# Performance work log

Measured on AMD Instinct MI355X. Metric: run time of the kernel, lower is better.

## Reference

```python
import jax, jax.numpy as jnp
import numpy as np
import math

B, S, D = 4096, 16, 256
HS, HT, O = 512, 512, 1


def setup_inputs() -> dict:
    key = jax.random.key(0)
    ks = jax.random.split(key, 20)
    stdv_s = 1.0 / math.sqrt(HS)
    stdv_t = 1.0 / math.sqrt(HT)
    u = lambda k, shape, s: jax.random.uniform(k, shape, jnp.float32, -s, s)
    return {
        "X": jax.random.normal(ks[0], (B, S, D), jnp.float32),
        # SpatialLSTM params (init uniform(-1/sqrt(H), 1/sqrt(H)) as in torch)
        "sa_W": u(ks[1], (D, 4 * HS), stdv_s),
        "sa_U": u(ks[2], (HS, 4 * HS), stdv_s),
        "sa_b": u(ks[3], (4 * HS,), stdv_s),
        "sa_Wa": u(ks[4], (D, D), stdv_s),
        "sa_Ua": u(ks[5], (2 * HS, D), stdv_s),
        "sa_ba": u(ks[6], (D,), stdv_s),
        "sa_Va": u(ks[7], (D, D), stdv_s),
        # TemporalLSTM params
        "ta_Wa": u(ks[8], (HS, S), stdv_t),
        "ta_Ua": u(ks[9], (HT, S), stdv_t),
        "ta_ba": u(ks[10], (S,), stdv_t),
        "ta_Va": u(ks[11], (S, S), stdv_t),
        "ta_W": u(ks[12], (HS, 4 * HT), stdv_t),
        "ta_U": u(ks[13], (HT, 4 * HT), stdv_t),
        "ta_b": u(ks[14], (4 * HT,), stdv_t),
        "ta_Wy": u(ks[15], (O, 4 * HT), stdv_t),
        "fc_W": u(ks[16], (O, HT), stdv_t),
        "fc_b": u(ks[17], (O,), stdv_t),
    }


def _lstm_update(gates, c, H):
    i = jax.nn.sigmoid(gates[:, :H])
    f = jax.nn.sigmoid(gates[:, H:2 * H])
    g = jnp.tanh(gates[:, 2 * H:3 * H])
    o = jax.nn.sigmoid(gates[:, 3 * H:])
    c_new = f * c + i * g
    h_new = o * jnp.tanh(c_new)
    return h_new, c_new


def _forward(X, sa_W, sa_U, sa_b, sa_Wa, sa_Ua, sa_ba, sa_Va,
             ta_Wa, ta_Ua, ta_ba, ta_Va, ta_W, ta_U, ta_b, ta_Wy, fc_W, fc_b):
    batch = X.shape[0]
    x = X  # x = X[:, :, 0:input_dim] == full X
    y0 = X[:, 0, D - 1:D]  # y = X[:, :, input_dim-1:], take t=0 -> [B, 1]

    # ---- Spatial attention LSTM over time ----
    def sa_step(carry, x_t):
        h, c = carry
        hc = jnp.concatenate([h, c], axis=1)  # [B, 2*HS]
        a_t = jnp.tanh(x_t @ sa_Wa + hc @ sa_Ua + sa_ba) @ sa_Va  # [B, D]
        alpha_t = jax.nn.softmax(a_t, axis=1)
        xt = alpha_t * x_t
        gates = xt @ sa_W + h @ sa_U + sa_b  # [B, 4*HS]
        h, c = _lstm_update(gates, c, HS)
        return (h, c), h

    h0 = jnp.zeros((batch, HS), X.dtype)
    c0 = jnp.zeros((batch, HS), X.dtype)
    _, hseq = jax.lax.scan(sa_step, (h0, c0), jnp.swapaxes(x, 0, 1))  # [S, B, HS]
    H3 = jnp.swapaxes(hseq, 0, 1)  # [B, S, HS]

    # ---- Temporal attention LSTM ----
    s0 = jnp.zeros((batch, HT), X.dtype)  # s_t is never updated in the original code

    def ta_step(carry, h_t):
        lh, lc, y_prev = carry
        beta = jnp.tanh(h_t @ ta_Wa + s0 @ ta_Ua + ta_ba) @ ta_Va  # [B, S]
        beta = jax.nn.softmax(beta, axis=1)
        h_ctx = jnp.einsum('bs,bsh->bh', beta, H3)  # [B, HS]
        gates = h_ctx @ ta_W + lh @ ta_U + y_prev @ ta_Wy + ta_b  # [B, 4*HT]
        lh, lc = _lstm_update(gates, lc, HT)
        y = lh @ fc_W.T + fc_b  # [B, O]
        return (lh, lc, y), None

    (_, _, y_pred), _ = jax.lax.scan(ta_step, (h0[:, :HT] * 0.0, c0[:, :HT] * 0.0, y0), hseq)
    return y_pred  # [B, O]


def reference(X, sa_W, sa_U, sa_b, sa_Wa, sa_Ua, sa_ba, sa_Va,
              ta_Wa, ta_Ua, ta_ba, ta_Va, ta_W, ta_U, ta_b, ta_Wy, fc_W, fc_b):
    return _forward(X, sa_W, sa_U, sa_b, sa_Wa, sa_Ua, sa_ba, sa_Va,
                    ta_Wa, ta_Ua, ta_ba, ta_Va, ta_W, ta_U, ta_b, ta_Wy, fc_W, fc_b)
```

## Files before the change

kernel.cpp:

```cpp
#include <hip/hip_runtime.h>


constexpr int Bb = 4096;
constexpr int Ss = 16;
constexpr int Dd = 256;
constexpr int Hh = 512;

typedef __attribute__((ext_vector_type(8))) short short8;
typedef __attribute__((ext_vector_type(4))) float f32x4;

__device__ __forceinline__ float sigm(float x) { return 1.0f / (1.0f + expf(-x)); }

__device__ __forceinline__ unsigned short f2bf(float x) {
    unsigned int u = __float_as_uint(x);
    u = (u + 0x7fffu + ((u >> 16) & 1u)) >> 16;
    return (unsigned short)u;
}
__device__ __forceinline__ float bf2f(unsigned short h) {
    return __uint_as_float(((unsigned int)h) << 16);
}
__device__ __forceinline__ void async16(const void* g, void* l) {
    __builtin_amdgcn_global_load_lds(
        (const __attribute__((address_space(1))) void*)g,
        (__attribute__((address_space(3))) void*)l, 16, 0, 0);
}

struct SegB { const unsigned short* Ah; const unsigned short* Al;
              const unsigned short* Bh; const unsigned short* Bl;
              int lda; int ldb; int K; };

template<int BM, int BN, int NSEG, int EPI>
__global__ __launch_bounds__(256) void gemm_mfma_k(
    SegB s0, SegB s1, SegB s2,
    const float* __restrict__ bias,
    float* __restrict__ C,
    unsigned short* __restrict__ Th, unsigned short* __restrict__ Tl,
    int ldc)
{
    constexpr int WM = BM / 2, WN = BN / 2;
    constexpr int FI = WM / 16, FJ = WN / 16;
    __shared__ __align__(16) unsigned short sA[2][BM * 32];
    __shared__ __align__(16) unsigned short sB[2][BN * 32];
    const int tid  = threadIdx.x;
    const int lane = tid & 63;
    const int wv   = tid >> 6;
    const int wm   = wv & 1, wn = wv >> 1;
    const int row0 = blockIdx.x * BM;
    const int col0 = blockIdx.y * BN;

    f32x4 acc[FI][FJ];
#pragma unroll
    for (int i = 0; i < FI; i++)
#pragma unroll
        for (int j = 0; j < FJ; j++) acc[i][j] = (f32x4){0.f, 0.f, 0.f, 0.f};

    const int lrow = lane >> 2;
    const int lcol = (lane & 3) * 8;
    const int q8   = (lane >> 4) * 8;
    const int l15  = lane & 15;

#pragma unroll
    for (int sgi = 0; sgi < NSEG; ++sgi) {
        const SegB sg = (sgi == 0) ? s0 : ((sgi == 1) ? s1 : s2);
        const int K = sg.K;
        for (int k0 = 0; k0 < K; k0 += 32) {
#pragma unroll
            for (int c = wv; c < BM / 16; c += 4) {
                const int r = c * 16 + lrow;
                const size_t gA = (size_t)(row0 + r) * sg.lda + k0 + lcol;
                const int lo = c * 512 + lane * 8;
                async16(sg.Ah + gA, &sA[0][lo]);
                async16(sg.Al + gA, &sA[1][lo]);
            }
#pragma unroll
            for (int c = wv; c < BN / 16; c += 4) {
                const int r = c * 16 + lrow;
                const size_t gB = (size_t)(col0 + r) * sg.ldb + k0 + lcol;
                const int lo = c * 512 + lane * 8;
                async16(sg.Bh + gB, &sB[0][lo]);
                async16(sg.Bl + gB, &sB[1][lo]);
            }
            __syncthreads();
            short8 ah[FI], al[FI], bh[FJ], bl[FJ];
#pragma unroll
            for (int i = 0; i < FI; i++) {
                const int m = wm * WM + i * 16 + l15;
                ah[i] = *reinterpret_cast<const short8*>(&sA[0][m * 32 + q8]);
                al[i] = *reinterpret_cast<const short8*>(&sA[1][m * 32 + q8]);
            }
#pragma unroll
            for (int j = 0; j < FJ; j++) {
                const int n = wn * WN + j * 16 + l15;
                bh[j] = *reinterpret_cast<const short8*>(&sB[0][n * 32 + q8]);
                bl[j] = *reinterpret_cast<const short8*>(&sB[1][n * 32 + q8]);
            }
#pragma unroll
            for (int i = 0; i < FI; i++)
#pragma unroll
                for (int j = 0; j < FJ; j++) {
                    acc[i][j] = __builtin_amdgcn_mfma_f32_16x16x32_bf16(ah[i], bh[j], acc[i][j], 0, 0, 0);
                    acc[i][j] = __builtin_amdgcn_mfma_f32_16x16x32_bf16(ah[i], bl[j], acc[i][j], 0, 0, 0);
                    acc[i][j] = __builtin_amdgcn_mfma_f32_16x16x32_bf16(al[i], bh[j], acc[i][j], 0, 0, 0);
                }
            __syncthreads();
        }
    }
#pragma unroll
    for (int i = 0; i < FI; i++) {
#pragma unroll
        for (int j = 0; j < FJ; j++) {
            const int col = col0 + wn * WN + j * 16 + l15;
#pragma unroll
            for (int r = 0; r < 4; r++) {
                const int row = row0 + wm * WM + i * 16 + (lane >> 4) * 4 + r;
                float v = acc[i][j][r];
                if (EPI == 1) {
                    v = tanhf(v + bias[col]);
                    unsigned short hb = f2bf(v);
                    Th[(size_t)row * ldc + col] = hb;
                    Tl[(size_t)row * ldc + col] = f2bf(v - bf2f(hb));
                } else {
                    C[(size_t)row * ldc + col] = v;
                }
            }
        }
    }
}

template<int NSEG, int ZC, int TA>
__global__ __launch_bounds__(256) void gemm_gates_k(
    SegB s0, SegB s1,
    const float* __restrict__ bias,
    const float* __restrict__ wy,
    const float* __restrict__ yv,
    float* __restrict__ c_io,
    unsigned short* __restrict__ hh, unsigned short* __restrict__ hl,
    unsigned short* __restrict__ ch, unsigned short* __restrict__ cl)
{
    __shared__ __align__(16) unsigned short sA[2][128 * 32];
    __shared__ __align__(16) unsigned short sB[2][128 * 32];
    const int tid  = threadIdx.x;
    const int lane = tid & 63;
    const int wv   = tid >> 6;
    const int wm   = wv & 1, wn = wv >> 1;
    const int row0 = blockIdx.x * 128;
    const int by32 = blockIdx.y * 32;

    f32x4 acc[4][4];
#pragma unroll
    for (int i = 0; i < 4; i++)
#pragma unroll
        for (int g = 0; g < 4; g++) acc[i][g] = (f32x4){0.f, 0.f, 0.f, 0.f};

    const int lrow = lane >> 2;
    const int lcol = (lane & 3) * 8;
    const int q8   = (lane >> 4) * 8;
    const int l15  = lane & 15;

#pragma unroll
    for (int sgi = 0; sgi < NSEG; ++sgi) {
        const SegB sg = (sgi == 0) ? s0 : s1;
        const int K = sg.K;
        for (int k0 = 0; k0 < K; k0 += 32) {
#pragma unroll
            for (int c = wv; c < 8; c += 4) {
                const int r = c * 16 + lrow;
                const size_t gA = (size_t)(row0 + r) * sg.lda + k0 + lcol;
                const int lo = c * 512 + lane * 8;
                async16(sg.Ah + gA, &sA[0][lo]);
                async16(sg.Al + gA, &sA[1][lo]);
            }
#pragma unroll
            for (int cc = wv; cc < 8; cc += 4) {
                const int g  = cc >> 1;
                const int jj = (cc & 1) * 16 + lrow;
                const int rowg = g * 512 + by32 + jj;
                const size_t gB = (size_t)rowg * sg.ldb + k0 + lcol;
                const int lo = cc * 512 + lane * 8;
                async16(sg.Bh + gB, &sB[0][lo]);
                async16(sg.Bl + gB, &sB[1][lo]);
            }
            __syncthreads();
            short8 ah[4], al[4], bh[4], bl[4];
#pragma unroll
            for (int i = 0; i < 4; i++) {
                const int m = wm * 64 + i * 16 + l15;
                ah[i] = *reinterpret_cast<const short8*>(&sA[0][m * 32 + q8]);
                al[i] = *reinterpret_cast<const short8*>(&sA[1][m * 32 + q8]);
            }
#pragma unroll
            for (int g = 0; g < 4; g++) {
                const int n = g * 32 + wn * 16 + l15;
                bh[g] = *reinterpret_cast<const short8*>(&sB[0][n * 32 + q8]);
                bl[g] = *reinterpret_cast<const short8*>(&sB[1][n * 32 + q8]);
            }
#pragma unroll
            for (int i = 0; i < 4; i++)
#pragma unroll
                for (int g = 0; g < 4; g++) {
                    acc[i][g] = __builtin_amdgcn_mfma_f32_16x16x32_bf16(ah[i], bh[g], acc[i][g], 0, 0, 0);
                    acc[i][g] = __builtin_amdgcn_mfma_f32_16x16x32_bf16(ah[i], bl[g], acc[i][g], 0, 0, 0);
                    acc[i][g] = __builtin_amdgcn_mfma_f32_16x16x32_bf16(al[i], bh[g], acc[i][g], 0, 0, 0);
                }
            __syncthreads();
        }
    }
    const int j = by32 + wn * 16 + l15;
    const float b0 = bias[j],            b1 = bias[Hh + j];
    const float b2 = bias[2 * Hh + j],   b3 = bias[3 * Hh + j];
    float w0 = 0.f, w1 = 0.f, w2 = 0.f, w3 = 0.f;
    if (TA) { w0 = wy[j]; w1 = wy[Hh + j]; w2 = wy[2 * Hh + j]; w3 = wy[3 * Hh + j]; }
#pragma unroll
    for (int i = 0; i < 4; i++) {
        const int rbase = row0 + wm * 64 + i * 16 + (lane >> 4) * 4;
#pragma unroll
        for (int r = 0; r < 4; r++) {
            const int row = rbase + r;
            float gi = acc[i][0][r] + b0;
            float gf = acc[i][1][r] + b1;
            float gg = acc[i][2][r] + b2;
            float go = acc[i][3][r] + b3;
            if (TA) {
                const float yb = yv[row];
                gi += yb * w0; gf += yb * w1; gg += yb * w2; go += yb * w3;
            }
            const float i_ = sigm(gi), f_ = sigm(gf), gv = tanhf(gg), o_ = sigm(go);
            const size_t idx = (size_t)row * Hh + j;
            const float cp = ZC ? 0.0f : c_io[idx];
            const float c = f_ * cp + i_ * gv;
            c_io[idx] = c;
            const float h = o_ * tanhf(c);
            const unsigned short hb = f2bf(h);
            hh[idx] = hb;
            hl[idx] = f2bf(h - bf2f(hb));
            if (!TA) {
                const unsigned short cb = f2bf(c);
                ch[idx] = cb;
                cl[idx] = f2bf(c - bf2f(cb));
            }
        }
    }
}

__global__ __launch_bounds__(256) void splitT_k(const float* __restrict__ W,
                                                unsigned short* __restrict__ Th,
                                                unsigned short* __restrict__ Tl,
                                                int Kd, int Nd)
{
    __shared__ float tile[32][33];
    const int bk = blockIdx.x * 32, bn = blockIdx.y * 32;
    const int tid = threadIdx.x;
    const int r = tid >> 3, c4 = (tid & 7) * 4;
    const float4 v = *reinterpret_cast<const float4*>(&W[(size_t)(bk + r) * Nd + bn + c4]);
    tile[r][c4 + 0] = v.x; tile[r][c4 + 1] = v.y;
    tile[r][c4 + 2] = v.z; tile[r][c4 + 3] = v.w;
    __syncthreads();
    const int n = r, k4 = c4;
    ushort4 hq, lq;
    unsigned short* hp = (unsigned short*)&hq;
    unsigned short* lp = (unsigned short*)&lq;
#pragma unroll
    for (int q = 0; q < 4; q++) {
        float x = tile[k4 + q][n];
        unsigned short h = f2bf(x);
        hp[q] = h;
        lp[q] = f2bf(x - bf2f(h));
    }
    *reinterpret_cast<ushort4*>(&Th[(size_t)(bn + n) * Kd + bk + k4]) = hq;
    *reinterpret_cast<ushort4*>(&Tl[(size_t)(bn + n) * Kd + bk + k4]) = lq;
}

__global__ __launch_bounds__(256) void splitWa_k(const float* __restrict__ W,
                                                 unsigned short* __restrict__ Th,
                                                 unsigned short* __restrict__ Tl)
{
    int idx = blockIdx.x * 256 + threadIdx.x;
    int n = idx >> 9, k = idx & 511;
    float x = W[(size_t)k * 16 + n];
    unsigned short h = f2bf(x);
    Th[idx] = h;
    Tl[idx] = f2bf(x - bf2f(h));
}

__global__ __launch_bounds__(256) void init_k(const float* __restrict__ X,
                                              unsigned short* __restrict__ xsh,
                                              unsigned short* __restrict__ xsl,
                                              float* __restrict__ yv)
{
    int idx = blockIdx.x * 256 + threadIdx.x;
    int b = idx >> 8, d = idx & 255;
    float xv = X[(size_t)b * (Ss * Dd) + d];
    unsigned short hb = f2bf(xv);
    xsh[idx] = hb;
    xsl[idx] = f2bf(xv - bf2f(hb));
    if (d == Dd - 1) yv[b] = xv;
}

template<int SPLITX>
__global__ __launch_bounds__(256) void softmax_xt_k(const float* __restrict__ a,
                                                    const float* __restrict__ X,
                                                    unsigned short* __restrict__ xh,
                                                    unsigned short* __restrict__ xl,
                                                    unsigned short* __restrict__ xsh,
                                                    unsigned short* __restrict__ xsl,
                                                    int t)
{
    int b = blockIdx.x, tid = threadIdx.x;
    __shared__ float red[256];
    float v = a[(size_t)b * Dd + tid];
    red[tid] = v; __syncthreads();
    for (int s = 128; s > 0; s >>= 1) {
        if (tid < s) red[tid] = fmaxf(red[tid], red[tid + s]);
        __syncthreads();
    }
    float mx = red[0]; __syncthreads();
    float e = expf(v - mx);
    red[tid] = e; __syncthreads();
    for (int s = 128; s > 0; s >>= 1) {
        if (tid < s) red[tid] += red[tid + s];
        __syncthreads();
    }
    float inv = 1.0f / red[0];
    float xv = e * inv * X[(size_t)b * Ss * Dd + (size_t)t * Dd + tid];
    unsigned short h = f2bf(xv);
    xh[(size_t)b * Dd + tid] = h;
    xl[(size_t)b * Dd + tid] = f2bf(xv - bf2f(h));
    if (SPLITX) {
        float xn = X[(size_t)b * Ss * Dd + (size_t)(t + 1) * Dd + tid];
        unsigned short xb = f2bf(xn);
        xsh[(size_t)b * Dd + tid] = xb;
        xsl[(size_t)b * Dd + tid] = f2bf(xn - bf2f(xb));
    }
}

__global__ __launch_bounds__(256) void beta_k(const unsigned short* __restrict__ H3h,
                                              const unsigned short* __restrict__ H3l,
                                              const unsigned short* __restrict__ WaTh,
                                              const unsigned short* __restrict__ WaTl,
                                              const float* __restrict__ taba,
                                              const float* __restrict__ taVa,
                                              float* __restrict__ beta)
{
    __shared__ __align__(16) unsigned short sW[2][16 * 512];
    __shared__ __align__(16) unsigned short sA[2][128 * 32];
    __shared__ float tt[128][17];
    __shared__ float Vas[256];
    const int tid  = threadIdx.x;
    const int lane = tid & 63;
    const int wv   = tid >> 6;
    const int lrow = lane >> 2;
    const int lcol = (lane & 3) * 8;
    const int q8   = (lane >> 4) * 8;
    const int l15  = lane & 15;
    const size_t row0 = (size_t)blockIdx.x * 128;

#pragma unroll
    for (int it = 0; it < 4; ++it) {
        const int lo = wv * 2048 + it * 512 + lane * 8;
        async16(WaTh + lo, &sW[0][lo]);
        async16(WaTl + lo, &sW[1][lo]);
    }
    Vas[tid] = taVa[tid];

    f32x4 acc[2];
    acc[0] = (f32x4){0.f, 0.f, 0.f, 0.f};
    acc[1] = (f32x4){0.f, 0.f, 0.f, 0.f};

    for (int kc = 0; kc < 16; ++kc) {
        const int k0 = kc * 32;
#pragma unroll
        for (int c = wv; c < 8; c += 4) {
            const int r = c * 16 + lrow;
            const size_t gA = (row0 + r) * Hh + k0 + lcol;
            const int lo = c * 512 + lane * 8;
            async16(H3h + gA, &sA[0][lo]);
            async16(H3l + gA, &sA[1][lo]);
        }
        __syncthreads();
        const short8 bh = *reinterpret_cast<const short8*>(&sW[0][l15 * 512 + k0 + q8]);
        const short8 bl = *reinterpret_cast<const short8*>(&sW[1][l15 * 512 + k0 + q8]);
#pragma unroll
        for (int i = 0; i < 2; i++) {
            const int m = wv * 32 + i * 16 + l15;
            const short8 ah = *reinterpret_cast<const short8*>(&sA[0][m * 32 + q8]);
            const short8 al = *reinterpret_cast<const short8*>(&sA[1][m * 32 + q8]);
            acc[i] = __builtin_amdgcn_mfma_f32_16x16x32_bf16(ah, bh, acc[i], 0, 0, 0);
            acc[i] = __builtin_amdgcn_mfma_f32_16x16x32_bf16(ah, bl, acc[i], 0, 0, 0);
            acc[i] = __builtin_amdgcn_mfma_f32_16x16x32_bf16(al, bh, acc[i], 0, 0, 0);
        }
        __syncthreads();
    }
    const float ba = taba[l15];
#pragma unroll
    for (int i = 0; i < 2; i++) {
#pragma unroll
        for (int r = 0; r < 4; r++) {
            const int rl = wv * 32 + i * 16 + (lane >> 4) * 4 + r;
            tt[rl][l15] = tanhf(acc[i][r] + ba);
        }
    }
    __syncthreads();
    if (tid < 128) {
        float tv[16];
#pragma unroll
        for (int m = 0; m < 16; m++) tv[m] = tt[tid][m];
        float l[16];
        float mx = -1e30f;
#pragma unroll
        for (int n = 0; n < 16; n++) {
            float s = 0.0f;
#pragma unroll
            for (int m = 0; m < 16; m++) s = fmaf(tv[m], Vas[m * 16 + n], s);
            l[n] = s;
            mx = fmaxf(mx, s);
        }
        float sum = 0.0f;
#pragma unroll
        for (int n = 0; n < 16; n++) { l[n] = expf(l[n] - mx); sum += l[n]; }
        const float inv = 1.0f / sum;
        float* bp = beta + (row0 + tid) * 16;
#pragma unroll
        for (int n4 = 0; n4 < 4; n4++) {
            float4 v = { l[n4 * 4] * inv, l[n4 * 4 + 1] * inv,
                         l[n4 * 4 + 2] * inv, l[n4 * 4 + 3] * inv };
            *reinterpret_cast<float4*>(bp + n4 * 4) = v;
        }
    }
}

__global__ __launch_bounds__(256) void hctx_all_k(unsigned short* __restrict__ H3h,
                                                  unsigned short* __restrict__ H3l,
                                                  const float* __restrict__ beta)
{
    const int b = blockIdx.x, tid = threadIdx.x;
    __shared__ float4 Hs4[16][129];
    __shared__ float bs[16][16];
    for (int i = tid; i < 16 * 128; i += 256) {
        const int s = i >> 7, q = i & 127;
        const size_t o = ((size_t)s * Bb + b) * Hh + q * 4;
        const ushort4 hv = *reinterpret_cast<const ushort4*>(&H3h[o]);
        const ushort4 lv = *reinterpret_cast<const ushort4*>(&H3l[o]);
        Hs4[s][q] = (float4){ bf2f(hv.x) + bf2f(lv.x), bf2f(hv.y) + bf2f(lv.y),
                              bf2f(hv.z) + bf2f(lv.z), bf2f(hv.w) + bf2f(lv.w) };
    }
    {
        const int t = tid >> 4, s = tid & 15;
        bs[t][s] = beta[((size_t)t * Bb + b) * 16 + s];
    }
    __syncthreads();
    const int q  = tid & 127;
    const int t0 = tid >> 7;
#pragma unroll
    for (int tt = 0; tt < 8; tt++) {
        const int t = tt * 2 + t0;
        float4 a = (float4){0.f, 0.f, 0.f, 0.f};
#pragma unroll
        for (int s = 0; s < 16; s++) {
            const float w = bs[t][s];
            const float4 hv = Hs4[s][q];
            a.x = fmaf(w, hv.x, a.x); a.y = fmaf(w, hv.y, a.y);
            a.z = fmaf(w, hv.z, a.z); a.w = fmaf(w, hv.w, a.w);
        }
        ushort4 ho, lo;
        ho.x = f2bf(a.x); lo.x = f2bf(a.x - bf2f(ho.x));
        ho.y = f2bf(a.y); lo.y = f2bf(a.y - bf2f(ho.y));
        ho.z = f2bf(a.z); lo.z = f2bf(a.z - bf2f(ho.z));
        ho.w = f2bf(a.w); lo.w = f2bf(a.w - bf2f(ho.w));
        const size_t o = ((size_t)t * Bb + b) * Hh + q * 4;
        *reinterpret_cast<ushort4*>(&H3h[o]) = ho;
        *reinterpret_cast<ushort4*>(&H3l[o]) = lo;
    }
}

__global__ __launch_bounds__(256) void y_k(const unsigned short* __restrict__ hh,
                                           const unsigned short* __restrict__ hl,
                                           const float* __restrict__ fcW,
                                           const float* __restrict__ fcb,
                                           float* __restrict__ yv,
                                           float* __restrict__ outp)
{
    int b = blockIdx.x, tid = threadIdx.x;
    size_t o = (size_t)b * Hh + tid;
    float h0 = bf2f(hh[o]) + bf2f(hl[o]);
    float h1 = bf2f(hh[o + 256]) + bf2f(hl[o + 256]);
    float p = h0 * fcW[tid] + h1 * fcW[tid + 256];
#pragma unroll
    for (int off = 32; off > 0; off >>= 1) p += __shfl_down(p, off, 64);
    __shared__ float wred[4];
    if ((tid & 63) == 0) wred[tid >> 6] = p;
    __syncthreads();
    if (tid == 0) {
        float y = fcb[0] + wred[0] + wred[1] + wred[2] + wred[3];
        yv[b] = y;
        if (outp) outp[b] = y;
    }
}

extern "C" void kernel_launch(void* const* d_in, const int* in_sizes, int n_in,
                              void* d_out, int out_size, void* d_ws, size_t ws_size,
                              hipStream_t stream)
{
    (void)in_sizes; (void)n_in; (void)out_size; (void)ws_size;
    const float* X     = (const float*)d_in[0];
    const float* sa_W  = (const float*)d_in[1];
    const float* sa_U  = (const float*)d_in[2];
    const float* sa_b  = (const float*)d_in[3];
    const float* sa_Wa = (const float*)d_in[4];
    const float* sa_Ua = (const float*)d_in[5];
    const float* sa_ba = (const float*)d_in[6];
    const float* sa_Va = (const float*)d_in[7];
    const float* ta_Wa = (const float*)d_in[8];
    const float* ta_ba = (const float*)d_in[10];
    const float* ta_Va = (const float*)d_in[11];
    const float* ta_W  = (const float*)d_in[12];
    const float* ta_U  = (const float*)d_in[13];
    const float* ta_b  = (const float*)d_in[14];
    const float* ta_Wy = (const float*)d_in[15];
    const float* fc_W  = (const float*)d_in[16];
    const float* fc_b  = (const float*)d_in[17];

    char* base = (char*)d_ws;
    size_t off = 0;
    auto alloc = [&](size_t bytes) {
        void* p = base + off; off += (bytes + 255) & ~(size_t)255; return p;
    };
    const size_t BH = (size_t)Bb * Hh;
    float* avxt = (float*)alloc((size_t)Bb * Dd * 4);
    unsigned short* H3h = (unsigned short*)alloc((size_t)Ss * BH * 2);
    unsigned short* H3l = (unsigned short*)alloc((size_t)Ss * BH * 2);
    float* cbuf = (float*)alloc(BH * 4);
    float* lc   = (float*)alloc(BH * 4);
    unsigned short* lhBh = (unsigned short*)alloc(BH * 2);
    unsigned short* lhBl = (unsigned short*)alloc(BH * 2);
    unsigned short* xth = (unsigned short*)alloc((size_t)Bb * Dd * 2);
    unsigned short* xtl = (unsigned short*)alloc((size_t)Bb * Dd * 2);
    unsigned short* xsh = (unsigned short*)alloc((size_t)Bb * Dd * 2);
    unsigned short* xsl = (unsigned short*)alloc((size_t)Bb * Dd * 2);
    unsigned short* ch  = (unsigned short*)alloc(BH * 2);
    unsigned short* cl  = (unsigned short*)alloc(BH * 2);
    unsigned short* tmph = (unsigned short*)alloc((size_t)Bb * Dd * 2);
    unsigned short* tmpl = (unsigned short*)alloc((size_t)Bb * Dd * 2);
    unsigned short* saWth = (unsigned short*)alloc((size_t)Dd * 4 * Hh * 2);
    unsigned short* saWtl = (unsigned short*)alloc((size_t)Dd * 4 * Hh * 2);
    unsigned short* saUth = (unsigned short*)alloc((size_t)Hh * 4 * Hh * 2);
    unsigned short* saUtl = (unsigned short*)alloc((size_t)Hh * 4 * Hh * 2);
    unsigned short* taWth = (unsigned short*)alloc((size_t)Hh * 4 * Hh * 2);
    unsigned short* taWtl = (unsigned short*)alloc((size_t)Hh * 4 * Hh * 2);
    unsigned short* taUth = (unsigned short*)alloc((size_t)Hh * 4 * Hh * 2);
    unsigned short* taUtl = (unsigned short*)alloc((size_t)Hh * 4 * Hh * 2);
    unsigned short* WaTh = (unsigned short*)alloc((size_t)Dd * Dd * 2);
    unsigned short* WaTl = (unsigned short*)alloc((size_t)Dd * Dd * 2);
    unsigned short* UaTh = (unsigned short*)alloc((size_t)2 * Hh * Dd * 2);
    unsigned short* UaTl = (unsigned short*)alloc((size_t)2 * Hh * Dd * 2);
    unsigned short* VaTh = (unsigned short*)alloc((size_t)Dd * Dd * 2);
    unsigned short* VaTl = (unsigned short*)alloc((size_t)Dd * Dd * 2);
    unsigned short* tWaTh = (unsigned short*)alloc((size_t)16 * Hh * 2);
    unsigned short* tWaTl = (unsigned short*)alloc((size_t)16 * Hh * 2);
    float* yv = (float*)alloc((size_t)Bb * 4);
    float* beta = (float*)xth;
    unsigned short* lhAh = (unsigned short*)cbuf;
    unsigned short* lhAl = (unsigned short*)cbuf + BH;
    unsigned short* lhh[2] = { lhAh, lhBh };
    unsigned short* lhl[2] = { lhAl, lhBl };

    splitT_k<<<dim3(Dd / 32, (4 * Hh) / 32), 256, 0, stream>>>(sa_W, saWth, saWtl, Dd, 4 * Hh);
    splitT_k<<<dim3(Hh / 32, (4 * Hh) / 32), 256, 0, stream>>>(sa_U, saUth, saUtl, Hh, 4 * Hh);
    splitT_k<<<dim3(Hh / 32, (4 * Hh) / 32), 256, 0, stream>>>(ta_W, taWth, taWtl, Hh, 4 * Hh);
    splitT_k<<<dim3(Hh / 32, (4 * Hh) / 32), 256, 0, stream>>>(ta_U, taUth, taUtl, Hh, 4 * Hh);
    splitT_k<<<dim3(Dd / 32, Dd / 32), 256, 0, stream>>>(sa_Wa, WaTh, WaTl, Dd, Dd);
    splitT_k<<<dim3((2 * Hh) / 32, Dd / 32), 256, 0, stream>>>(sa_Ua, UaTh, UaTl, 2 * Hh, Dd);
    splitT_k<<<dim3(Dd / 32, Dd / 32), 256, 0, stream>>>(sa_Va, VaTh, VaTl, Dd, Dd);
    splitWa_k<<<dim3(32), 256, 0, stream>>>(ta_Wa, tWaTh, tWaTl);
    init_k<<<dim3((Bb * Dd) / 256), 256, 0, stream>>>(X, xsh, xsl, yv);

    const dim3 agrid(Bb / 32, Dd / 64);
    const dim3 ggrid(Bb / 128, Hh / 32);

    for (int t = 0; t < Ss; ++t) {
        SegB a0{ xsh, xsl, WaTh, WaTl, Dd, Dd, Dd };
        if (t == 0) {
            gemm_mfma_k<32, 64, 1, 1><<<agrid, 256, 0, stream>>>(
                a0, a0, a0, sa_ba, nullptr, tmph, tmpl, Dd);
        } else {
            SegB a1{ H3h + (size_t)(t - 1) * BH, H3l + (size_t)(t - 1) * BH,
                     UaTh, UaTl, Hh, 2 * Hh, Hh };
            SegB a2{ ch, cl, UaTh + Hh, UaTl + Hh, Hh, 2 * Hh, Hh };
            gemm_mfma_k<32, 64, 3, 1><<<agrid, 256, 0, stream>>>(
                a0, a1, a2, sa_ba, nullptr, tmph, tmpl, Dd);
        }

        SegB v0{ tmph, tmpl, VaTh, VaTl, Dd, Dd, Dd };
        gemm_mfma_k<32, 64, 1, 0><<<agrid, 256, 0, stream>>>(
            v0, v0, v0, nullptr, avxt, nullptr, nullptr, Dd);

        if (t < Ss - 1)
            softmax_xt_k<1><<<Bb, 256, 0, stream>>>(avxt, X, xth, xtl, xsh, xsl, t);
        else
            softmax_xt_k<0><<<Bb, 256, 0, stream>>>(avxt, X, xth, xtl, xsh, xsl, t);

        SegB g0{ xth, xtl, saWth, saWtl, Dd, Dd, Dd };
        if (t == 0) {
            gemm_gates_k<1, 1, 0><<<ggrid, 256, 0, stream>>>(
                g0, g0, sa_b, nullptr, nullptr, cbuf,
                H3h + (size_t)t * BH, H3l + (size_t)t * BH, ch, cl);
        } else {
            SegB g1{ H3h + (size_t)(t - 1) * BH, H3l + (size_t)(t - 1) * BH,
                     saUth, saUtl, Hh, Hh, Hh };
            gemm_gates_k<2, 0, 0><<<ggrid, 256, 0, stream>>>(
                g0, g1, sa_b, nullptr, nullptr, cbuf,
                H3h + (size_t)t * BH, H3l + (size_t)t * BH, ch, cl);
        }
    }

    beta_k<<<dim3((Ss * Bb) / 128), 256, 0, stream>>>(
        H3h, H3l, tWaTh, tWaTl, ta_ba, ta_Va, beta);
    hctx_all_k<<<Bb, 256, 0, stream>>>(H3h, H3l, beta);

    for (int t = 0; t < Ss; ++t) {
        SegB g0{ H3h + (size_t)t * BH, H3l + (size_t)t * BH,
                 taWth, taWtl, Hh, Hh, Hh };
        const int po = t & 1;
        if (t == 0) {
            gemm_gates_k<1, 1, 1><<<ggrid, 256, 0, stream>>>(
                g0, g0, ta_b, ta_Wy, yv, lc, lhh[0], lhl[0], nullptr, nullptr);
        } else {
            SegB g1{ lhh[(t - 1) & 1], lhl[(t - 1) & 1], taUth, taUtl, Hh, Hh, Hh };
            gemm_gates_k<2, 0, 1><<<ggrid, 256, 0, stream>>>(
                g0, g1, ta_b, ta_Wy, yv, lc, lhh[po], lhl[po], nullptr, nullptr);
        }
        y_k<<<Bb, 256, 0, stream>>>(lhh[po], lhl[po], fc_W, fc_b, yv,
                                    (t == Ss - 1) ? (float*)d_out : nullptr);
    }
}
```

Before: 2.413 ms.

## Fuse spatial attention GEMMs and softmax into one per-row-block kernel

Replaces the two attention GEMM launches and the separate softmax/x-scaling kernel with a single kernel per time step. Each block of 16 batch rows computes the tanh projection, stages it in LDS, multiplies by Va, and runs the row softmax and the scaling by x_t in LDS. This removes the global round trips of the tmp and logits buffers and two launches per step. In exchange, operands are read straight from global memory without LDS staging or prefetch, and the grid shrinks to 256 blocks, which may leave the GEMM portion latency-bound.

```diff
diff --git a/kernel.cpp b/kernel.cpp
--- a/kernel.cpp
+++ b/kernel.cpp
@@ -24,105 +24,161 @@
         (const __attribute__((address_space(1))) void*)g,
         (__attribute__((address_space(3))) void*)l, 16, 0, 0);
 }
+__device__ __forceinline__ short8 ldg8(const unsigned short* p) {
+    return *reinterpret_cast<const short8*>(p);
+}
 
 struct SegB { const unsigned short* Ah; const unsigned short* Al;
               const unsigned short* Bh; const unsigned short* Bl;
               int lda; int ldb; int K; };
 
-template<int BM, int BN, int NSEG, int EPI>
-__global__ __launch_bounds__(256) void gemm_mfma_k(
+template<int NSEG, int SPLITX>
+__global__ __launch_bounds__(256) void attn_fused_k(
     SegB s0, SegB s1, SegB s2,
-    const float* __restrict__ bias,
-    float* __restrict__ C,
-    unsigned short* __restrict__ Th, unsigned short* __restrict__ Tl,
-    int ldc)
-{
-    constexpr int WM = BM / 2, WN = BN / 2;
-    constexpr int FI = WM / 16, FJ = WN / 16;
-    __shared__ __align__(16) unsigned short sA[2][BM * 32];
-    __shared__ __align__(16) unsigned short sB[2][BN * 32];
+    const unsigned short* __restrict__ VaTh, const unsigned short* __restrict__ VaTl,
+    const float* __restrict__ saba,
+    const float* __restrict__ X, int t,
+    unsigned short* __restrict__ xth, unsigned short* __restrict__ xtl,
+    unsigned short* __restrict__ xsh, unsigned short* __restrict__ xsl)
+{
+    __shared__ __align__(16) unsigned short tmpH[16 * 264];
+    __shared__ __align__(16) unsigned short tmpL[16 * 264];
+    __shared__ __align__(16) float av[16 * 260];
+    __shared__ float rpart[16][16];
+    __shared__ float spart[16][16];
+
     const int tid  = threadIdx.x;
     const int lane = tid & 63;
     const int wv   = tid >> 6;
-    const int wm   = wv & 1, wn = wv >> 1;
-    const int row0 = blockIdx.x * BM;
-    const int col0 = blockIdx.y * BN;
-
-    f32x4 acc[FI][FJ];
-#pragma unroll
-    for (int i = 0; i < FI; i++)
-#pragma unroll
-        for (int j = 0; j < FJ; j++) acc[i][j] = (f32x4){0.f, 0.f, 0.f, 0.f};
-
-    const int lrow = lane >> 2;
-    const int lcol = (lane & 3) * 8;
     const int q8   = (lane >> 4) * 8;
     const int l15  = lane & 15;
+    const int quad = lane >> 4;
+    const int row0 = blockIdx.x * 16;
+
+    f32x4 acc[4];
+#pragma unroll
+    for (int j = 0; j < 4; j++) acc[j] = (f32x4){0.f, 0.f, 0.f, 0.f};
 
 #pragma unroll
     for (int sgi = 0; sgi < NSEG; ++sgi) {
         const SegB sg = (sgi == 0) ? s0 : ((sgi == 1) ? s1 : s2);
-        const int K = sg.K;
-        for (int k0 = 0; k0 < K; k0 += 32) {
-#pragma unroll
-            for (int c = wv; c < BM / 16; c += 4) {
-                const int r = c * 16 + lrow;
-                const size_t gA = (size_t)(row0 + r) * sg.lda + k0 + lcol;
-                const int lo = c * 512 + lane * 8;
-                async16(sg.Ah + gA, &sA[0][lo]);
-                async16(sg.Al + gA, &sA[1][lo]);
+        for (int k0 = 0; k0 < sg.K; k0 += 32) {
+            const size_t aoff = (size_t)(row0 + l15) * sg.lda + k0 + q8;
+            const short8 a_h = ldg8(sg.Ah + aoff);
+            const short8 a_l = ldg8(sg.Al + aoff);
+#pragma unroll
+            for (int j = 0; j < 4; j++) {
+                const int n = wv * 64 + j * 16 + l15;
+                const size_t boff = (size_t)n * sg.ldb + k0 + q8;
+                const short8 b_h = ldg8(sg.Bh + boff);
+                const short8 b_l = ldg8(sg.Bl + boff);
+                acc[j] = __builtin_amdgcn_mfma_f32_16x16x32_bf16(a_h, b_h, acc[j], 0, 0, 0);
+                acc[j] = __builtin_amdgcn_mfma_f32_16x16x32_bf16(a_h, b_l, acc[j], 0, 0, 0);
+                acc[j] = __builtin_amdgcn_mfma_f32_16x16x32_bf16(a_l, b_h, acc[j], 0, 0, 0);
             }
-#pragma unroll
-            for (int c = wv; c < BN / 16; c += 4) {
-                const int r = c * 16 + lrow;
-                const size_t gB = (size_t)(col0 + r) * sg.ldb + k0 + lcol;
-                const int lo = c * 512 + lane * 8;
-                async16(sg.Bh + gB, &sB[0][lo]);
-                async16(sg.Bl + gB, &sB[1][lo]);
-            }
-            __syncthreads();
-            short8 ah[FI], al[FI], bh[FJ], bl[FJ];
-#pragma unroll
-            for (int i = 0; i < FI; i++) {
-                const int m = wm * WM + i * 16 + l15;
-                ah[i] = *reinterpret_cast<const short8*>(&sA[0][m * 32 + q8]);
-                al[i] = *reinterpret_cast<const short8*>(&sA[1][m * 32 + q8]);
-            }
-#pragma unroll
-            for (int j = 0; j < FJ; j++) {
-                const int n = wn * WN + j * 16 + l15;
-                bh[j] = *reinterpret_cast<const short8*>(&sB[0][n * 32 + q8]);
-                bl[j] = *reinterpret_cast<const short8*>(&sB[1][n * 32 + q8]);
-            }
-#pragma unroll
-            for (int i = 0; i < FI; i++)
-#pragma unroll
-                for (int j = 0; j < FJ; j++) {
-                    acc[i][j] = __builtin_amdgcn_mfma_f32_16x16x32_bf16(ah[i], bh[j], acc[i][j], 0, 0, 0);
-                    acc[i][j] = __builtin_amdgcn_mfma_f32_16x16x32_bf16(ah[i], bl[j], acc[i][j], 0, 0, 0);
-                    acc[i][j] = __builtin_amdgcn_mfma_f32_16x16x32_bf16(al[i], bh[j], acc[i][j], 0, 0, 0);
-                }
-            __syncthreads();
-        }
-    }
-#pragma unroll
-    for (int i = 0; i < FI; i++) {
-#pragma unroll
-        for (int j = 0; j < FJ; j++) {
-            const int col = col0 + wn * WN + j * 16 + l15;
-#pragma unroll
-            for (int r = 0; r < 4; r++) {
-                const int row = row0 + wm * WM + i * 16 + (lane >> 4) * 4 + r;
-                float v = acc[i][j][r];
-                if (EPI == 1) {
-                    v = tanhf(v + bias[col]);
-                    unsigned short hb = f2bf(v);
-                    Th[(size_t)row * ldc + col] = hb;
-                    Tl[(size_t)row * ldc + col] = f2bf(v - bf2f(hb));
-                } else {
-                    C[(size_t)row * ldc + col] = v;
-                }
-            }
+        }
+    }
+#pragma unroll
+    for (int j = 0; j < 4; j++) {
+        const int col = wv * 64 + j * 16 + l15;
+        const float bb = saba[col];
+#pragma unroll
+        for (int r = 0; r < 4; r++) {
+            const int rw = quad * 4 + r;
+            const float v = tanhf(acc[j][r] + bb);
+            const unsigned short hb = f2bf(v);
+            tmpH[rw * 264 + col] = hb;
+            tmpL[rw * 264 + col] = f2bf(v - bf2f(hb));
+        }
+    }
+    __syncthreads();
+
+    f32x4 acc2[4];
+#pragma unroll
+    for (int j = 0; j < 4; j++) acc2[j] = (f32x4){0.f, 0.f, 0.f, 0.f};
+#pragma unroll
+    for (int kc = 0; kc < 8; ++kc) {
+        const int k0 = kc * 32;
+        const short8 a_h = *reinterpret_cast<const short8*>(&tmpH[l15 * 264 + k0 + q8]);
+        const short8 a_l = *reinterpret_cast<const short8*>(&tmpL[l15 * 264 + k0 + q8]);
+#pragma unroll
+        for (int j = 0; j < 4; j++) {
+            const int n = wv * 64 + j * 16 + l15;
+            const size_t boff = (size_t)n * 256 + k0 + q8;
+            const short8 b_h = ldg8(VaTh + boff);
+            const short8 b_l = ldg8(VaTl + boff);
+            acc2[j] = __builtin_amdgcn_mfma_f32_16x16x32_bf16(a_h, b_h, acc2[j], 0, 0, 0);
+            acc2[j] = __builtin_amdgcn_mfma_f32_16x16x32_bf16(a_h, b_l, acc2[j], 0, 0, 0);
+            acc2[j] = __builtin_amdgcn_mfma_f32_16x16x32_bf16(a_l, b_h, acc2[j], 0, 0, 0);
+        }
+    }
+#pragma unroll
+    for (int j = 0; j < 4; j++) {
+        const int col = wv * 64 + j * 16 + l15;
+#pragma unroll
+        for (int r = 0; r < 4; r++) av[(quad * 4 + r) * 260 + col] = acc2[j][r];
+    }
+    __syncthreads();
+
+    const int row = tid >> 4;
+    const int sl  = tid & 15;
+    const int c0  = sl * 16;
+    float* avr = av + row * 260;
+    float mx = avr[c0];
+#pragma unroll
+    for (int i = 1; i < 16; i++) mx = fmaxf(mx, avr[c0 + i]);
+    rpart[row][sl] = mx;
+    __syncthreads();
+    float M = rpart[row][0];
+#pragma unroll
+    for (int i = 1; i < 16; i++) M = fmaxf(M, rpart[row][i]);
+    float s = 0.0f;
+#pragma unroll
+    for (int i = 0; i < 16; i++) {
+        const float e = expf(avr[c0 + i] - M);
+        avr[c0 + i] = e;
+        s += e;
+    }
+    spart[row][sl] = s;
+    __syncthreads();
+    float S = spart[row][0];
+#pragma unroll
+    for (int i = 1; i < 16; i++) S += spart[row][i];
+    const float inv = 1.0f / S;
+
+    const size_t b = (size_t)(row0 + row);
+    const float* Xr = X + b * (Ss * Dd) + (size_t)t * Dd + c0;
+    unsigned short* xhp = xth + b * Dd + c0;
+    unsigned short* xlp = xtl + b * Dd + c0;
+#pragma unroll
+    for (int g = 0; g < 4; g++) {
+        const float4 xv = *reinterpret_cast<const float4*>(Xr + g * 4);
+        const float v0 = avr[c0 + g * 4 + 0] * inv * xv.x;
+        const float v1 = avr[c0 + g * 4 + 1] * inv * xv.y;
+        const float v2 = avr[c0 + g * 4 + 2] * inv * xv.z;
+        const float v3 = avr[c0 + g * 4 + 3] * inv * xv.w;
+        ushort4 ho, lo;
+        ho.x = f2bf(v0); lo.x = f2bf(v0 - bf2f(ho.x));
+        ho.y = f2bf(v1); lo.y = f2bf(v1 - bf2f(ho.y));
+        ho.z = f2bf(v2); lo.z = f2bf(v2 - bf2f(ho.z));
+        ho.w = f2bf(v3); lo.w = f2bf(v3 - bf2f(ho.w));
+        *reinterpret_cast<ushort4*>(xhp + g * 4) = ho;
+        *reinterpret_cast<ushort4*>(xlp + g * 4) = lo;
+    }
+    if (SPLITX) {
+        const float* Xn = X + b * (Ss * Dd) + (size_t)(t + 1) * Dd + c0;
+        unsigned short* shp = xsh + b * Dd + c0;
+        unsigned short* slp = xsl + b * Dd + c0;
+#pragma unroll
+        for (int g = 0; g < 4; g++) {
+            const float4 xv = *reinterpret_cast<const float4*>(Xn + g * 4);
+            ushort4 ho, lo;
+            ho.x = f2bf(xv.x); lo.x = f2bf(xv.x - bf2f(ho.x));
+            ho.y = f2bf(xv.y); lo.y = f2bf(xv.y - bf2f(ho.y));
+            ho.z = f2bf(xv.z); lo.z = f2bf(xv.z - bf2f(ho.z));
+            ho.w = f2bf(xv.w); lo.w = f2bf(xv.w - bf2f(ho.w));
+            *reinterpret_cast<ushort4*>(shp + g * 4) = ho;
+            *reinterpret_cast<ushort4*>(slp + g * 4) = lo;
         }
     }
 }
@@ -296,43 +352,6 @@
     if (d == Dd - 1) yv[b] = xv;
 }
 
-template<int SPLITX>
-__global__ __launch_bounds__(256) void softmax_xt_k(const float* __restrict__ a,
-                                                    const float* __restrict__ X,
-                                                    unsigned short* __restrict__ xh,
-                                                    unsigned short* __restrict__ xl,
-                                                    unsigned short* __restrict__ xsh,
-                                                    unsigned short* __restrict__ xsl,
-                                                    int t)
-{
-    int b = blockIdx.x, tid = threadIdx.x;
-    __shared__ float red[256];
-    float v = a[(size_t)b * Dd + tid];
-    red[tid] = v; __syncthreads();
-    for (int s = 128; s > 0; s >>= 1) {
-        if (tid < s) red[tid] = fmaxf(red[tid], red[tid + s]);
-        __syncthreads();
-    }
-    float mx = red[0]; __syncthreads();
-    float e = expf(v - mx);
-    red[tid] = e; __syncthreads();
-    for (int s = 128; s > 0; s >>= 1) {
-        if (tid < s) red[tid] += red[tid + s];
-        __syncthreads();
-    }
-    float inv = 1.0f / red[0];
-    float xv = e * inv * X[(size_t)b * Ss * Dd + (size_t)t * Dd + tid];
-    unsigned short h = f2bf(xv);
-    xh[(size_t)b * Dd + tid] = h;
-    xl[(size_t)b * Dd + tid] = f2bf(xv - bf2f(h));
-    if (SPLITX) {
-        float xn = X[(size_t)b * Ss * Dd + (size_t)(t + 1) * Dd + tid];
-        unsigned short xb = f2bf(xn);
-        xsh[(size_t)b * Dd + tid] = xb;
-        xsl[(size_t)b * Dd + tid] = f2bf(xn - bf2f(xb));
-    }
-}
-
 __global__ __launch_bounds__(256) void beta_k(const unsigned short* __restrict__ H3h,
                                               const unsigned short* __restrict__ H3l,
                                               const unsigned short* __restrict__ WaTh,
@@ -525,7 +544,6 @@
         void* p = base + off; off += (bytes + 255) & ~(size_t)255; return p;
     };
     const size_t BH = (size_t)Bb * Hh;
-    float* avxt = (float*)alloc((size_t)Bb * Dd * 4);
     unsigned short* H3h = (unsigned short*)alloc((size_t)Ss * BH * 2);
     unsigned short* H3l = (unsigned short*)alloc((size_t)Ss * BH * 2);
     float* cbuf = (float*)alloc(BH * 4);
@@ -538,8 +556,6 @@
     unsigned short* xsl = (unsigned short*)alloc((size_t)Bb * Dd * 2);
     unsigned short* ch  = (unsigned short*)alloc(BH * 2);
     unsigned short* cl  = (unsigned short*)alloc(BH * 2);
-    unsigned short* tmph = (unsigned short*)alloc((size_t)Bb * Dd * 2);
-    unsigned short* tmpl = (unsigned short*)alloc((size_t)Bb * Dd * 2);
     unsigned short* saWth = (unsigned short*)alloc((size_t)Dd * 4 * Hh * 2);
     unsigned short* saWtl = (unsigned short*)alloc((size_t)Dd * 4 * Hh * 2);
     unsigned short* saUth = (unsigned short*)alloc((size_t)Hh * 4 * Hh * 2);
@@ -573,30 +589,25 @@
     splitWa_k<<<dim3(32), 256, 0, stream>>>(ta_Wa, tWaTh, tWaTl);
     init_k<<<dim3((Bb * Dd) / 256), 256, 0, stream>>>(X, xsh, xsl, yv);
 
-    const dim3 agrid(Bb / 32, Dd / 64);
+    const dim3 agrid(Bb / 16);
     const dim3 ggrid(Bb / 128, Hh / 32);
 
     for (int t = 0; t < Ss; ++t) {
         SegB a0{ xsh, xsl, WaTh, WaTl, Dd, Dd, Dd };
         if (t == 0) {
-            gemm_mfma_k<32, 64, 1, 1><<<agrid, 256, 0, stream>>>(
-                a0, a0, a0, sa_ba, nullptr, tmph, tmpl, Dd);
+            attn_fused_k<1, 1><<<agrid, 256, 0, stream>>>(
+                a0, a0, a0, VaTh, VaTl, sa_ba, X, t, xth, xtl, xsh, xsl);
         } else {
             SegB a1{ H3h + (size_t)(t - 1) * BH, H3l + (size_t)(t - 1) * BH,
                      UaTh, UaTl, Hh, 2 * Hh, Hh };
             SegB a2{ ch, cl, UaTh + Hh, UaTl + Hh, Hh, 2 * Hh, Hh };
-            gemm_mfma_k<32, 64, 3, 1><<<agrid, 256, 0, stream>>>(
-                a0, a1, a2, sa_ba, nullptr, tmph, tmpl, Dd);
-        }
-
-        SegB v0{ tmph, tmpl, VaTh, VaTl, Dd, Dd, Dd };
-        gemm_mfma_k<32, 64, 1, 0><<<agrid, 256, 0, stream>>>(
-            v0, v0, v0, nullptr, avxt, nullptr, nullptr, Dd);
-
-        if (t < Ss - 1)
-            softmax_xt_k<1><<<Bb, 256, 0, stream>>>(avxt, X, xth, xtl, xsh, xsl, t);
-        else
-            softmax_xt_k<0><<<Bb, 256, 0, stream>>>(avxt, X, xth, xtl, xsh, xsl, t);
+            if (t < Ss - 1)
+                attn_fused_k<3, 1><<<agrid, 256, 0, stream>>>(
+                    a0, a1, a2, VaTh, VaTl, sa_ba, X, t, xth, xtl, xsh, xsl);
+            else
+                attn_fused_k<3, 0><<<agrid, 256, 0, stream>>>(
+                    a0, a1, a2, VaTh, VaTl, sa_ba, X, t, xth, xtl, xsh, xsl);
+        }
 
         SegB g0{ xth, xtl, saWth, saWtl, Dd, Dd, Dd };
         if (t == 0) {
```

Result: slower. 3.010 ms (+24.8%).

## Fuse attention Va GEMM with softmax and x_t scaling into one kernel

Applied to the files above, without the earlier changes.

Replaces the separate Va projection GEMM and per-row softmax kernel with a single kernel that computes a 16-row by 256-column tile of tanh(...)@Va using MFMA with split-bf16 precision, keeps the scores in shared memory, and applies softmax, the X scaling and the hi/lo bf16 split in place. This removes the fp32 score buffer round trip through global memory and one kernel launch per timestep. It also replaces a tree reduction with many barriers per row by a 16-lane partial reduction. The trade-off is that each block reloads the whole Va matrix with only 16 rows of reuse, and the grid shrinks to 256 blocks.

```diff
diff --git a/kernel.cpp b/kernel.cpp
--- a/kernel.cpp
+++ b/kernel.cpp
@@ -23,6 +23,9 @@
     __builtin_amdgcn_global_load_lds(
         (const __attribute__((address_space(1))) void*)g,
         (__attribute__((address_space(3))) void*)l, 16, 0, 0);
+}
+__device__ __forceinline__ short8 ldg8(const unsigned short* p) {
+    return *reinterpret_cast<const short8*>(p);
 }
 
 struct SegB { const unsigned short* Ah; const unsigned short* Al;
@@ -123,6 +126,135 @@
                     C[(size_t)row * ldc + col] = v;
                 }
             }
+        }
+    }
+}
+
+template<int SPLITX>
+__global__ __launch_bounds__(256) void a2sm_k(
+    const unsigned short* __restrict__ tmph, const unsigned short* __restrict__ tmpl,
+    const unsigned short* __restrict__ VaTh, const unsigned short* __restrict__ VaTl,
+    const float* __restrict__ X, int t,
+    unsigned short* __restrict__ xth, unsigned short* __restrict__ xtl,
+    unsigned short* __restrict__ xsh, unsigned short* __restrict__ xsl)
+{
+    __shared__ __align__(16) unsigned short sB[2][256 * 32];
+    __shared__ __align__(16) float av[16 * 260];
+    __shared__ float rpart[16][16];
+    __shared__ float spart[16][16];
+
+    const int tid  = threadIdx.x;
+    const int lane = tid & 63;
+    const int wv   = tid >> 6;
+    const int q8   = (lane >> 4) * 8;
+    const int l15  = lane & 15;
+    const int quad = lane >> 4;
+    const int lrow = lane >> 2;
+    const int lcol = (lane & 3) * 8;
+    const int row0 = blockIdx.x * 16;
+
+    short8 a_h[8], a_l[8];
+#pragma unroll
+    for (int kc = 0; kc < 8; kc++) {
+        const size_t aoff = (size_t)(row0 + l15) * 256 + kc * 32 + q8;
+        a_h[kc] = ldg8(tmph + aoff);
+        a_l[kc] = ldg8(tmpl + aoff);
+    }
+
+    f32x4 acc[4];
+#pragma unroll
+    for (int j = 0; j < 4; j++) acc[j] = (f32x4){0.f, 0.f, 0.f, 0.f};
+
+    for (int kc = 0; kc < 8; ++kc) {
+        const int k0 = kc * 32;
+#pragma unroll
+        for (int c = wv; c < 16; c += 4) {
+            const int n = c * 16 + lrow;
+            const size_t gB = (size_t)n * 256 + k0 + lcol;
+            const int lo = c * 512 + lane * 8;
+            async16(VaTh + gB, &sB[0][lo]);
+            async16(VaTl + gB, &sB[1][lo]);
+        }
+        __syncthreads();
+#pragma unroll
+        for (int j = 0; j < 4; j++) {
+            const int n = wv * 64 + j * 16 + l15;
+            const short8 b_h = *reinterpret_cast<const short8*>(&sB[0][n * 32 + q8]);
+            const short8 b_l = *reinterpret_cast<const short8*>(&sB[1][n * 32 + q8]);
+            acc[j] = __builtin_amdgcn_mfma_f32_16x16x32_bf16(a_h[kc], b_h, acc[j], 0, 0, 0);
+            acc[j] = __builtin_amdgcn_mfma_f32_16x16x32_bf16(a_h[kc], b_l, acc[j], 0, 0, 0);
+            acc[j] = __builtin_amdgcn_mfma_f32_16x16x32_bf16(a_l[kc], b_h, acc[j], 0, 0, 0);
+        }
+        __syncthreads();
+    }
+
+#pragma unroll
+    for (int j = 0; j < 4; j++) {
+        const int col = wv * 64 + j * 16 + l15;
+#pragma unroll
+        for (int r = 0; r < 4; r++) av[(quad * 4 + r) * 260 + col] = acc[j][r];
+    }
+    __syncthreads();
+
+    const int row = tid >> 4;
+    const int sl  = tid & 15;
+    const int c0  = sl * 16;
+    float* avr = av + row * 260;
+    float mx = avr[c0];
+#pragma unroll
+    for (int i = 1; i < 16; i++) mx = fmaxf(mx, avr[c0 + i]);
+    rpart[row][sl] = mx;
+    __syncthreads();
+    float M = rpart[row][0];
+#pragma unroll
+    for (int i = 1; i < 16; i++) M = fmaxf(M, rpart[row][i]);
+    float s = 0.0f;
+#pragma unroll
+    for (int i = 0; i < 16; i++) {
+        const float e = expf(avr[c0 + i] - M);
+        avr[c0 + i] = e;
+        s += e;
+    }
+    spart[row][sl] = s;
+    __syncthreads();
+    float S = spart[row][0];
+#pragma unroll
+    for (int i = 1; i < 16; i++) S += spart[row][i];
+    const float inv = 1.0f / S;
+
+    const size_t b = (size_t)(row0 + row);
+    const float* Xr = X + b * (Ss * Dd) + (size_t)t * Dd + c0;
+    unsigned short* xhp = xth + b * Dd + c0;
+    unsigned short* xlp = xtl + b * Dd + c0;
+#pragma unroll
+    for (int g = 0; g < 4; g++) {
+        const float4 xv = *reinterpret_cast<const float4*>(Xr + g * 4);
+        const float v0 = avr[c0 + g * 4 + 0] * inv * xv.x;
+        const float v1 = avr[c0 + g * 4 + 1] * inv * xv.y;
+        const float v2 = avr[c0 + g * 4 + 2] * inv * xv.z;
+        const float v3 = avr[c0 + g * 4 + 3] * inv * xv.w;
+        ushort4 ho, lo;
+        ho.x = f2bf(v0); lo.x = f2bf(v0 - bf2f(ho.x));
+        ho.y = f2bf(v1); lo.y = f2bf(v1 - bf2f(ho.y));
+        ho.z = f2bf(v2); lo.z = f2bf(v2 - bf2f(ho.z));
+        ho.w = f2bf(v3); lo.w = f2bf(v3 - bf2f(ho.w));
+        *reinterpret_cast<ushort4*>(xhp + g * 4) = ho;
+        *reinterpret_cast<ushort4*>(xlp + g * 4) = lo;
+    }
+    if (SPLITX) {
+        const float* Xn = X + b * (Ss * Dd) + (size_t)(t + 1) * Dd + c0;
+        unsigned short* shp = xsh + b * Dd + c0;
+        unsigned short* slp = xsl + b * Dd + c0;
+#pragma unroll
+        for (int g = 0; g < 4; g++) {
+            const float4 xv = *reinterpret_cast<const float4*>(Xn + g * 4);
+            ushort4 ho, lo;
+            ho.x = f2bf(xv.x); lo.x = f2bf(xv.x - bf2f(ho.x));
+            ho.y = f2bf(xv.y); lo.y = f2bf(xv.y - bf2f(ho.y));
+            ho.z = f2bf(xv.z); lo.z = f2bf(xv.z - bf2f(ho.z));
+            ho.w = f2bf(xv.w); lo.w = f2bf(xv.w - bf2f(ho.w));
+            *reinterpret_cast<ushort4*>(shp + g * 4) = ho;
+            *reinterpret_cast<ushort4*>(slp + g * 4) = lo;
         }
     }
 }
@@ -294,43 +426,6 @@
     xsh[idx] = hb;
     xsl[idx] = f2bf(xv - bf2f(hb));
     if (d == Dd - 1) yv[b] = xv;
-}
-
-template<int SPLITX>
-__global__ __launch_bounds__(256) void softmax_xt_k(const float* __restrict__ a,
-                                                    const float* __restrict__ X,
-                                                    unsigned short* __restrict__ xh,
-                                                    unsigned short* __restrict__ xl,
-                                                    unsigned short* __restrict__ xsh,
-                                                    unsigned short* __restrict__ xsl,
-                                                    int t)
-{
-    int b = blockIdx.x, tid = threadIdx.x;
-    __shared__ float red[256];
-    float v = a[(size_t)b * Dd + tid];
-    red[tid] = v; __syncthreads();
-    for (int s = 128; s > 0; s >>= 1) {
-        if (tid < s) red[tid] = fmaxf(red[tid], red[tid + s]);
-        __syncthreads();
-    }
-    float mx = red[0]; __syncthreads();
-    float e = expf(v - mx);
-    red[tid] = e; __syncthreads();
-    for (int s = 128; s > 0; s >>= 1) {
-        if (tid < s) red[tid] += red[tid + s];
-        __syncthreads();
-    }
-    float inv = 1.0f / red[0];
-    float xv = e * inv * X[(size_t)b * Ss * Dd + (size_t)t * Dd + tid];
-    unsigned short h = f2bf(xv);
-    xh[(size_t)b * Dd + tid] = h;
-    xl[(size_t)b * Dd + tid] = f2bf(xv - bf2f(h));
-    if (SPLITX) {
-        float xn = X[(size_t)b * Ss * Dd + (size_t)(t + 1) * Dd + tid];
-        unsigned short xb = f2bf(xn);
-        xsh[(size_t)b * Dd + tid] = xb;
-        xsl[(size_t)b * Dd + tid] = f2bf(xn - bf2f(xb));
-    }
 }
 
 __global__ __launch_bounds__(256) void beta_k(const unsigned short* __restrict__ H3h,
@@ -525,7 +620,6 @@
         void* p = base + off; off += (bytes + 255) & ~(size_t)255; return p;
     };
     const size_t BH = (size_t)Bb * Hh;
-    float* avxt = (float*)alloc((size_t)Bb * Dd * 4);
     unsigned short* H3h = (unsigned short*)alloc((size_t)Ss * BH * 2);
     unsigned short* H3l = (unsigned short*)alloc((size_t)Ss * BH * 2);
     float* cbuf = (float*)alloc(BH * 4);
@@ -574,6 +668,7 @@
     init_k<<<dim3((Bb * Dd) / 256), 256, 0, stream>>>(X, xsh, xsl, yv);
 
     const dim3 agrid(Bb / 32, Dd / 64);
+    const dim3 smgrid(Bb / 16);
     const dim3 ggrid(Bb / 128, Hh / 32);
 
     for (int t = 0; t < Ss; ++t) {
@@ -589,14 +684,12 @@
                 a0, a1, a2, sa_ba, nullptr, tmph, tmpl, Dd);
         }
 
-        SegB v0{ tmph, tmpl, VaTh, VaTl, Dd, Dd, Dd };
-        gemm_mfma_k<32, 64, 1, 0><<<agrid, 256, 0, stream>>>(
-            v0, v0, v0, nullptr, avxt, nullptr, nullptr, Dd);
-
         if (t < Ss - 1)
-            softmax_xt_k<1><<<Bb, 256, 0, stream>>>(avxt, X, xth, xtl, xsh, xsl, t);
+            a2sm_k<1><<<smgrid, 256, 0, stream>>>(
+                tmph, tmpl, VaTh, VaTl, X, t, xth, xtl, xsh, xsl);
         else
-            softmax_xt_k<0><<<Bb, 256, 0, stream>>>(avxt, X, xth, xtl, xsh, xsl, t);
+            a2sm_k<0><<<smgrid, 256, 0, stream>>>(
+                tmph, tmpl, VaTh, VaTl, X, t, xth, xtl, xsh, xsl);
 
         SegB g0{ xth, xtl, saWth, saWtl, Dd, Dd, Dd };
         if (t == 0) {
```

New measurement: 2.400 ms. About the same (-0.5%).
